# Optimization experiments

Hardware: AMD Instinct MI355X
Metric: run time of the kernel (lower is better)

Reference implementation:

```python
import jax, jax.numpy as jnp
import numpy as np

ORI = 10        # orientation bins
PPC = 8         # pixels_per_cell
CPB = 2         # cells_per_block
MAX_ANGLE = float(np.pi)
EPS = 1e-5


def _sobel_weight():
    m = jnp.array([[1., 0., -1.], [2., 0., -2.], [1., 0., -1.]], dtype=jnp.float32)
    return jnp.stack([m, m.T])[:, None]  # (2, 1, 3, 3): [gx-like, gy-like]


def setup_inputs() -> dict:
    key = jax.random.key(0)
    img = jax.random.uniform(key, (16, 1, 512, 512), dtype=jnp.float32)
    return {"img": img, "weight": _sobel_weight()}


def reference(img, weight):
    # Sobel-pair conv, stride 1, padding 1 -> (N, 2, H, W)
    gxy = jax.lax.conv_general_dilated(
        img, weight, window_strides=(1, 1), padding=((1, 1), (1, 1)),
        dimension_numbers=("NCHW", "OIHW", "NCHW"))
    mag = jnp.linalg.norm(gxy, axis=1)                    # (N, H, W)
    phase = jnp.arctan2(gxy[:, 0], gxy[:, 1])             # (N, H, W)
    p = phase / MAX_ANGLE * ORI
    f = jnp.mod(jnp.floor(p).astype(jnp.int32), ORI)
    c = jnp.mod(jnp.ceil(p).astype(jnp.int32), ORI)
    # scatter_(floor, mag) then scatter_add_(ceil, 1-mag) on a zero tensor
    # == one_hot(floor)*mag + one_hot(ceil)*(1-mag)  (each pixel writes one bin)
    out = (jax.nn.one_hot(f, ORI, axis=1, dtype=mag.dtype) * mag[:, None]
           + jax.nn.one_hot(c, ORI, axis=1, dtype=mag.dtype) * (1.0 - mag)[:, None])
    N, O, H, W = out.shape
    hc, wc = H // PPC, W // PPC
    # cell average pool (exact 8x8, no padding)
    cells = out.reshape(N, O, hc, PPC, wc, PPC).mean(axis=(3, 5))  # (N, O, hc, wc)
    nbr, nbc = hc - CPB + 1, wc - CPB + 1
    # unfold(2,CPB,1).unfold(3,CPB,1) -> (N, O, nbr, nbc, CPB, CPB)
    blk = jnp.stack([
        jnp.stack([cells[:, :, di:di + nbr, dj:dj + nbc] for dj in range(CPB)], axis=-1)
        for di in range(CPB)], axis=-2)
    # faithful 'L2' branch: divide by sqrt((sum over block)^2 + eps^2)
    denom = jnp.sqrt(blk.sum(axis=(-1, -2)) ** 2 + EPS ** 2)[..., None, None]
    blk = blk / denom
    return blk.reshape(N, -1)  # feature_vector=True
```

## Files before the change

### kernel.cpp

```cpp
#include <hip/hip_runtime.h>
#include <math.h>

#define NIMG 16
#define HP 512
#define WP 512
#define ORI 10
#define RS 68
#define RAWN (34 * RS)

__global__ __launch_bounds__(256, 6) void hog_cells_k(const float* __restrict__ img,
                                                      float* __restrict__ cells) {
    __shared__ float raw[RAWN];
    __shared__ float hist[32 * 11];
    const int n   = blockIdx.z;
    const int by  = blockIdx.y;
    const int bx  = blockIdx.x;
    const int ty0 = by * 32;
    const int tx0 = bx * 64;
    const float* im = img + (size_t)n * (HP * WP);
    const int tid = threadIdx.x;

    if (by == 0  && tid < RS) raw[tid] = 0.0f;
    if (by == 15 && tid < RS) raw[33 * RS + tid] = 0.0f;
    if (bx == 0 && tid < 34) raw[tid * RS] = 0.0f;
    if (bx == 7 && tid < 34) raw[tid * RS + 65] = 0.0f;

#if __has_builtin(__builtin_amdgcn_raw_ptr_buffer_load_lds) && __has_builtin(__builtin_amdgcn_make_buffer_rsrc)
    {
        auto rsrc = __builtin_amdgcn_make_buffer_rsrc((void*)im, (short)0,
                                                      HP * WP * 4, 0x00020000);
        const int wv = tid >> 6;
        #pragma unroll
        for (int k = 0; k < 10; ++k) {
            int e = k * 256 + tid;
            int r = e / RS;
            int c = e - r * RS;
            int gcol = tx0 + c - 1;
            bool colok = ((unsigned)gcol < (unsigned)WP);
            int voff = ((ty0 + r - 1) * WP + gcol) * 4;
            if (e < RAWN && colok) {
                __builtin_amdgcn_raw_ptr_buffer_load_lds(
                    rsrc,
                    (__attribute__((address_space(3))) void*)&raw[k * 256 + wv * 64],
                    4, voff, 0, 0, 0);
            }
        }
    }
#else
    for (int e = tid; e < RAWN; e += 256) {
        int r = e / RS, c = e - r * RS;
        int grow = ty0 + r - 1, gcol = tx0 + c - 1;
        bool ok = ((unsigned)grow < (unsigned)HP) && ((unsigned)gcol < (unsigned)WP);
        raw[e] = ok ? im[grow * WP + gcol] : 0.0f;
    }
#endif
    __syncthreads();

    const int cell = tid >> 3;
    const int sub  = tid & 7;
    const int ccy = cell >> 3, ccx = cell & 7;
    const int pr = ccy * 8 + sub;
    const int cb = ccx * 8;

    const int b0 = pr * RS + cb;
    float4 a0 = *(const float4*)&raw[b0],          a1 = *(const float4*)&raw[b0 + 4],
           a2 = *(const float4*)&raw[b0 + 8];
    float4 bb0 = *(const float4*)&raw[b0 + RS],    bb1 = *(const float4*)&raw[b0 + RS + 4],
           bb2 = *(const float4*)&raw[b0 + RS + 8];
    float4 c0 = *(const float4*)&raw[b0 + 2 * RS], c1 = *(const float4*)&raw[b0 + 2 * RS + 4],
           c2 = *(const float4*)&raw[b0 + 2 * RS + 8];
    const float A[12] = {a0.x,a0.y,a0.z,a0.w, a1.x,a1.y,a1.z,a1.w, a2.x,a2.y,a2.z,a2.w};
    const float B[12] = {bb0.x,bb0.y,bb0.z,bb0.w, bb1.x,bb1.y,bb1.z,bb1.w, bb2.x,bb2.y,bb2.z,bb2.w};
    const float C[12] = {c0.x,c0.y,c0.z,c0.w, c1.x,c1.y,c1.z,c1.w, c2.x,c2.y,c2.z,c2.w};

    float t[10], u[10];
    #pragma unroll
    for (int j = 0; j < 10; ++j) {
        t[j] = A[j] + 2.0f * B[j] + C[j];
        u[j] = A[j] - C[j];
    }

    float T[11];
    #pragma unroll
    for (int j = 0; j < 11; ++j) T[j] = 0.0f;

    #pragma unroll
    for (int j = 0; j < 8; ++j) {
        float gx = t[j] - t[j+2];
        float gy = u[j] + 2.0f * u[j+1] + u[j+2];
        float mag = __builtin_amdgcn_sqrtf(gx * gx + gy * gy);
        float wB = 1.0f - mag;
        bool gx0 = (gx == 0.0f);
        bool gy0 = (gy == 0.0f);
        if (gx0 | gy0) wB = 0.0f;
        float yv = fabsf(gx);
        float xv = (gx < 0.0f) ? -gy : gy;
        if (gx0) xv = 1.0f;
        float y1 = yv * 0.9510565163f, y2 = yv * 0.8090169944f,
              y3 = yv * 0.5877852523f, y4 = yv * 0.3090169944f;
        float x1 = xv * 0.3090169944f, x2 = xv * 0.5877852523f,
              x3 = xv * 0.8090169944f, x4 = xv * 0.9510565163f;
        bool e1 = (y1 >= x1), e2 = (y2 >= x2), e3 = (y3 >= x3), e4 = (y4 >= x4);
        bool e5 = (xv <= 0.0f);
        bool e6 = (y4 <= -x4), e7 = (y3 <= -x3), e8 = (y2 <= -x2), e9 = (y1 <= -x1);
        T[0]  += 1.0f;
        T[1]  += e1 ? 1.0f : wB;
        T[2]  += e2 ? 1.0f : (e1 ? wB : 0.0f);
        T[3]  += e3 ? 1.0f : (e2 ? wB : 0.0f);
        T[4]  += e4 ? 1.0f : (e3 ? wB : 0.0f);
        T[5]  += e5 ? 1.0f : (e4 ? wB : 0.0f);
        T[6]  += e6 ? 1.0f : (e5 ? wB : 0.0f);
        T[7]  += e7 ? 1.0f : (e6 ? wB : 0.0f);
        T[8]  += e8 ? 1.0f : (e7 ? wB : 0.0f);
        T[9]  += e9 ? 1.0f : (e8 ? wB : 0.0f);
        T[10] += e9 ? wB : 0.0f;
    }

    float b[10];
    #pragma unroll
    for (int j = 0; j < 10; ++j) b[j] = T[j] - T[j + 1];
    b[0] += T[10];
    #pragma unroll
    for (int j = 0; j < 10; ++j) {
        float v = b[j];
        v += __shfl_xor(v, 1);
        v += __shfl_xor(v, 2);
        v += __shfl_xor(v, 4);
        b[j] = v;
    }
    if (sub == 0) {
        #pragma unroll
        for (int j = 0; j < 10; ++j) hist[cell * 11 + j] = b[j];
    }
    __syncthreads();

    const int gcy0 = by * 4;
    const int gcx0 = bx * 8;
    for (int i = tid; i < 32 * ORI; i += 256) {
        int bn = i >> 5;
        int cl = i & 31;
        int cyy = cl >> 3, cxx = cl & 7;
        cells[(((size_t)n * ORI + bn) * 64 + gcy0 + cyy) * 64 + (gcx0 + cxx)]
            = hist[cl * 11 + bn] * 0.015625f;
    }
}

__global__ __launch_bounds__(256) void hog_blocks_k(const float* __restrict__ cells,
                                                    float* __restrict__ out) {
    const int total = NIMG * ORI * 63 * 63;
    int idx = blockIdx.x * blockDim.x + threadIdx.x;
    if (idx >= total) return;
    int bc = idx % 63;
    int t  = idx / 63;
    int br = t % 63;
    int no = t / 63;
    const float* c = cells + (((size_t)no * 64 + br) * 64 + bc);
    float c00 = c[0], c01 = c[1], c10 = c[64], c11 = c[65];
    float s = ((c00 + c01) + (c10 + c11));
    float denom = sqrtf(s * s + 1e-10f);
    float inv = 1.0f / denom;
    float4 o;
    o.x = c00 * inv;
    o.y = c01 * inv;
    o.z = c10 * inv;
    o.w = c11 * inv;
    reinterpret_cast<float4*>(out)[idx] = o;
}

extern "C" void kernel_launch(void* const* d_in, const int* in_sizes, int n_in,
                              void* d_out, int out_size, void* d_ws, size_t ws_size,
                              hipStream_t stream) {
    (void)in_sizes; (void)n_in; (void)out_size; (void)ws_size;
    const float* img = (const float*)d_in[0];
    float* out   = (float*)d_out;
    float* cells = (float*)d_ws;

    hog_cells_k<<<dim3(8, 16, NIMG), 256, 0, stream>>>(img, cells);

    const int total = NIMG * ORI * 63 * 63;
    hog_blocks_k<<<(total + 255) / 256, 256, 0, stream>>>(cells, out);
}
```

Before: 22.04 us.

## Process two row tiles per block with double-buffered LDS staging

Each block now handles two vertically adjacent 32x64 tiles. It issues the async global-to-LDS loads for the second tile while computing the histogram of the first, to hide load latency. It also vectorises the Sobel row sums with float4 and replaces the constant T[0] accumulation with a literal. The trade-off is half as many blocks and double the LDS per block, which lowers occupancy and the parallelism available on the GPU.

```diff
diff --git a/kernel.cpp b/kernel.cpp
--- a/kernel.cpp
+++ b/kernel.cpp
@@ -8,86 +8,70 @@
 #define RS 68
 #define RAWN (34 * RS)
 
-__global__ __launch_bounds__(256, 6) void hog_cells_k(const float* __restrict__ img,
-                                                      float* __restrict__ cells) {
-    __shared__ float raw[RAWN];
-    __shared__ float hist[32 * 11];
-    const int n   = blockIdx.z;
-    const int by  = blockIdx.y;
-    const int bx  = blockIdx.x;
-    const int ty0 = by * 32;
+__device__ __forceinline__ void stage_tile(const float* __restrict__ im,
+                                           float* rawbuf, int tyIdx, int bx,
+                                           int tid) {
+    const int ty0 = tyIdx * 32;
     const int tx0 = bx * 64;
-    const float* im = img + (size_t)n * (HP * WP);
-    const int tid = threadIdx.x;
-
-    if (by == 0  && tid < RS) raw[tid] = 0.0f;
-    if (by == 15 && tid < RS) raw[33 * RS + tid] = 0.0f;
-    if (bx == 0 && tid < 34) raw[tid * RS] = 0.0f;
-    if (bx == 7 && tid < 34) raw[tid * RS + 65] = 0.0f;
-
+    if (tyIdx == 0  && tid < RS) rawbuf[tid] = 0.0f;
+    if (tyIdx == 15 && tid < RS) rawbuf[33 * RS + tid] = 0.0f;
+    if (bx == 0 && tid < 34) rawbuf[tid * RS] = 0.0f;
+    if (bx == 7 && tid < 34) rawbuf[tid * RS + 65] = 0.0f;
 #if __has_builtin(__builtin_amdgcn_raw_ptr_buffer_load_lds) && __has_builtin(__builtin_amdgcn_make_buffer_rsrc)
-    {
-        auto rsrc = __builtin_amdgcn_make_buffer_rsrc((void*)im, (short)0,
-                                                      HP * WP * 4, 0x00020000);
-        const int wv = tid >> 6;
-        #pragma unroll
-        for (int k = 0; k < 10; ++k) {
-            int e = k * 256 + tid;
-            int r = e / RS;
-            int c = e - r * RS;
-            int gcol = tx0 + c - 1;
-            bool colok = ((unsigned)gcol < (unsigned)WP);
-            int voff = ((ty0 + r - 1) * WP + gcol) * 4;
-            if (e < RAWN && colok) {
-                __builtin_amdgcn_raw_ptr_buffer_load_lds(
-                    rsrc,
-                    (__attribute__((address_space(3))) void*)&raw[k * 256 + wv * 64],
-                    4, voff, 0, 0, 0);
-            }
-        }
+    auto rsrc = __builtin_amdgcn_make_buffer_rsrc((void*)im, (short)0,
+                                                  HP * WP * 4, 0x00020000);
+    const int wv = tid >> 6;
+    #pragma unroll
+    for (int k = 0; k < 10; ++k) {
+        int e = k * 256 + tid;
+        int r = e / RS, c = e - r * RS;
+        int gcol = tx0 + c - 1;
+        bool colok = ((unsigned)gcol < (unsigned)WP);
+        int voff = ((ty0 + r - 1) * WP + gcol) * 4;
+        if (e < RAWN && colok)
+            __builtin_amdgcn_raw_ptr_buffer_load_lds(
+                rsrc,
+                (__attribute__((address_space(3))) void*)&rawbuf[k * 256 + wv * 64],
+                4, voff, 0, 0, 0);
     }
 #else
     for (int e = tid; e < RAWN; e += 256) {
         int r = e / RS, c = e - r * RS;
         int grow = ty0 + r - 1, gcol = tx0 + c - 1;
         bool ok = ((unsigned)grow < (unsigned)HP) && ((unsigned)gcol < (unsigned)WP);
-        raw[e] = ok ? im[grow * WP + gcol] : 0.0f;
+        rawbuf[e] = ok ? im[(size_t)grow * WP + gcol] : 0.0f;
     }
 #endif
-    __syncthreads();
+}
 
+__device__ __forceinline__ void compute_tile(const float* rawbuf, float* hist,
+                                             int tid) {
     const int cell = tid >> 3;
     const int sub  = tid & 7;
     const int ccy = cell >> 3, ccx = cell & 7;
     const int pr = ccy * 8 + sub;
-    const int cb = ccx * 8;
+    const float4* r4 = (const float4*)rawbuf;
+    const int s = pr * 17 + ccx * 2;
+    float4 A0 = r4[s],      A1 = r4[s + 1],  A2 = r4[s + 2];
+    float4 B0 = r4[s + 17], B1 = r4[s + 18], B2 = r4[s + 19];
+    float4 C0 = r4[s + 34], C1 = r4[s + 35], C2 = r4[s + 36];
 
-    const int b0 = pr * RS + cb;
-    float4 a0 = *(const float4*)&raw[b0],          a1 = *(const float4*)&raw[b0 + 4],
-           a2 = *(const float4*)&raw[b0 + 8];
-    float4 bb0 = *(const float4*)&raw[b0 + RS],    bb1 = *(const float4*)&raw[b0 + RS + 4],
-           bb2 = *(const float4*)&raw[b0 + RS + 8];
-    float4 c0 = *(const float4*)&raw[b0 + 2 * RS], c1 = *(const float4*)&raw[b0 + 2 * RS + 4],
-           c2 = *(const float4*)&raw[b0 + 2 * RS + 8];
-    const float A[12] = {a0.x,a0.y,a0.z,a0.w, a1.x,a1.y,a1.z,a1.w, a2.x,a2.y,a2.z,a2.w};
-    const float B[12] = {bb0.x,bb0.y,bb0.z,bb0.w, bb1.x,bb1.y,bb1.z,bb1.w, bb2.x,bb2.y,bb2.z,bb2.w};
-    const float C[12] = {c0.x,c0.y,c0.z,c0.w, c1.x,c1.y,c1.z,c1.w, c2.x,c2.y,c2.z,c2.w};
-
-    float t[10], u[10];
-    #pragma unroll
-    for (int j = 0; j < 10; ++j) {
-        t[j] = A[j] + 2.0f * B[j] + C[j];
-        u[j] = A[j] - C[j];
-    }
+    float4 t4a = A0 + 2.0f * B0 + C0, t4b = A1 + 2.0f * B1 + C1,
+           t4c = A2 + 2.0f * B2 + C2;
+    float4 u4a = A0 - C0, u4b = A1 - C1, u4c = A2 - C2;
+    const float t[12] = {t4a.x,t4a.y,t4a.z,t4a.w, t4b.x,t4b.y,t4b.z,t4b.w,
+                         t4c.x,t4c.y,t4c.z,t4c.w};
+    const float u[12] = {u4a.x,u4a.y,u4a.z,u4a.w, u4b.x,u4b.y,u4b.z,u4b.w,
+                         u4c.x,u4c.y,u4c.z,u4c.w};
 
     float T[11];
     #pragma unroll
-    for (int j = 0; j < 11; ++j) T[j] = 0.0f;
+    for (int j = 1; j < 11; ++j) T[j] = 0.0f;
 
     #pragma unroll
     for (int j = 0; j < 8; ++j) {
-        float gx = t[j] - t[j+2];
-        float gy = u[j] + 2.0f * u[j+1] + u[j+2];
+        float gx = t[j] - t[j + 2];
+        float gy = u[j] + 2.0f * u[j + 1] + u[j + 2];
         float mag = __builtin_amdgcn_sqrtf(gx * gx + gy * gy);
         float wB = 1.0f - mag;
         bool gx0 = (gx == 0.0f);
@@ -103,7 +87,6 @@
         bool e1 = (y1 >= x1), e2 = (y2 >= x2), e3 = (y3 >= x3), e4 = (y4 >= x4);
         bool e5 = (xv <= 0.0f);
         bool e6 = (y4 <= -x4), e7 = (y3 <= -x3), e8 = (y2 <= -x2), e9 = (y1 <= -x1);
-        T[0]  += 1.0f;
         T[1]  += e1 ? 1.0f : wB;
         T[2]  += e2 ? 1.0f : (e1 ? wB : 0.0f);
         T[3]  += e3 ? 1.0f : (e2 ? wB : 0.0f);
@@ -117,9 +100,9 @@
     }
 
     float b[10];
+    b[0] = 8.0f - T[1] + T[10];
     #pragma unroll
-    for (int j = 0; j < 10; ++j) b[j] = T[j] - T[j + 1];
-    b[0] += T[10];
+    for (int j = 1; j < 10; ++j) b[j] = T[j] - T[j + 1];
     #pragma unroll
     for (int j = 0; j < 10; ++j) {
         float v = b[j];
@@ -132,17 +115,42 @@
         #pragma unroll
         for (int j = 0; j < 10; ++j) hist[cell * 11 + j] = b[j];
     }
-    __syncthreads();
+}
 
-    const int gcy0 = by * 4;
+__device__ __forceinline__ void writeout_tile(float* __restrict__ cells,
+                                              const float* hist, int n,
+                                              int tyIdx, int bx, int tid) {
+    const int gcy0 = tyIdx * 4;
     const int gcx0 = bx * 8;
     for (int i = tid; i < 32 * ORI; i += 256) {
         int bn = i >> 5;
         int cl = i & 31;
-        int cyy = cl >> 3, cxx = cl & 7;
-        cells[(((size_t)n * ORI + bn) * 64 + gcy0 + cyy) * 64 + (gcx0 + cxx)]
+        cells[(((size_t)n * ORI + bn) * 64 + gcy0 + (cl >> 3)) * 64 + gcx0 + (cl & 7)]
             = hist[cl * 11 + bn] * 0.015625f;
     }
+}
+
+__global__ __launch_bounds__(256, 4) void hog_cells_k(const float* __restrict__ img,
+                                                      float* __restrict__ cells) {
+    __shared__ __align__(16) float raw[2][RAWN];
+    __shared__ float hist[32 * 11];
+    const int n   = blockIdx.z;
+    const int bx  = blockIdx.x;
+    const int byp = blockIdx.y;
+    const int tyA = byp * 2, tyB = tyA + 1;
+    const float* im = img + (size_t)n * (HP * WP);
+    const int tid = threadIdx.x;
+
+    stage_tile(im, raw[0], tyA, bx, tid);
+    __syncthreads();
+    stage_tile(im, raw[1], tyB, bx, tid);
+    compute_tile(raw[0], hist, tid);
+    __syncthreads();
+    writeout_tile(cells, hist, n, tyA, bx, tid);
+    __syncthreads();
+    compute_tile(raw[1], hist, tid);
+    __syncthreads();
+    writeout_tile(cells, hist, n, tyB, bx, tid);
 }
 
 __global__ __launch_bounds__(256) void hog_blocks_k(const float* __restrict__ cells,
@@ -175,7 +183,7 @@
     float* out   = (float*)d_out;
     float* cells = (float*)d_ws;
 
-    hog_cells_k<<<dim3(8, 16, NIMG), 256, 0, stream>>>(img, cells);
+    hog_cells_k<<<dim3(8, 8, NIMG), 256, 0, stream>>>(img, cells);
 
     const int total = NIMG * ORI * 63 * 63;
     hog_blocks_k<<<(total + 255) / 256, 256, 0, stream>>>(cells, out);
```

Measured after the change: 21.69 us. About the same (-1.6%).
